# Kernel tuning notes

Measured on AMD Instinct MI355X. Metric: run time of the kernel, lower is better.

The kernel has to match this reference:

```python
import jax, jax.numpy as jnp
import numpy as np

NEG_INF = -1e30  # stand-in for -inf that is safe under fp16/bf16 softmax


def setup_inputs() -> dict:
    key = jax.random.key(0)
    k1, k2, k3, k4 = jax.random.split(key, 4)
    B, S, D_IN, D_OUT = 4, 4096, 2048, 2048
    x = jax.random.normal(k1, (B, S, D_IN), dtype=jnp.float32)
    scale = 0.02
    Wq = jax.random.normal(k2, (D_IN, D_OUT), dtype=jnp.float32) * scale
    Wk = jax.random.normal(k3, (D_IN, D_OUT), dtype=jnp.float32) * scale
    Wv = jax.random.normal(k4, (D_IN, D_OUT), dtype=jnp.float32) * scale
    return {"x": x, "Wq": Wq, "Wk": Wk, "Wv": Wv}


def reference(x, Wq, Wk, Wv):
    # x: [B, S, d_in]; Wq/Wk/Wv: [d_in, d_out] (torch Linear weight transposed)
    B, S, _ = x.shape
    q = jnp.einsum('bsd,de->bse', x, Wq)
    k = jnp.einsum('bsd,de->bse', x, Wk)
    v = jnp.einsum('bsd,de->bse', x, Wv)
    d_k = k.shape[-1]
    scale = 1.0 / jnp.sqrt(jnp.asarray(d_k, dtype=x.dtype))
    # attn_scores[b, i, j] = q_i . k_j
    scores = jnp.einsum('bqe,bke->bqk', q, k) * scale
    # causal mask: position i attends to j <= i
    i = jnp.arange(S)[:, None]
    j = jnp.arange(S)[None, :]
    scores = jnp.where(j > i, NEG_INF, scores)
    attn = jax.nn.softmax(scores, axis=-1)
    # dropout p=0.0 / eval mode -> identity
    return jnp.einsum('bqk,bke->bqe', attn, v)
```

## Files before the change

### kernel.cpp

```cpp
#include <hip/hip_runtime.h>

using u16   = unsigned short;
using s16x8 = __attribute__((ext_vector_type(8))) short;
using u16x8 = __attribute__((ext_vector_type(8))) unsigned short;
using f32x4 = __attribute__((ext_vector_type(4))) float;

__device__ __forceinline__ u16 f2bf(float f) {
    unsigned u = __float_as_uint(f);
    u += 0x7FFFu + ((u >> 16) & 1u);
    return (u16)(u >> 16);
}

__device__ __forceinline__ void gload16(const void* g, void* l) {
    __builtin_amdgcn_global_load_lds((const __attribute__((address_space(1))) void*)g,
                                     (__attribute__((address_space(3))) void*)l, 16, 0, 0);
}

#define MFMA_BF16(a, b, d) \
    d = __builtin_amdgcn_mfma_f32_16x16x32_bf16(a, b, d, 0, 0, 0)

__device__ __forceinline__ void gemm256_core(
    const u16* __restrict__ A, const u16* __restrict__ Bt,
    int lda, int ldb, int kSteps, u16* lds, f32x4 (&acc)[8][4])
{
    const int tid  = threadIdx.x;
    const int lane = tid & 63;
    const int wid  = tid >> 6;
    const int wr   = wid >> 2;
    const int wc   = wid & 3;
    const int c    = lane & 15;
    const int g    = lane >> 4;

    const int srow = tid >> 3;
    const int scol = ((tid & 7) * 8) ^ ((srow & 7) << 3);
    const u16* pA = A  + (size_t)srow * lda + scol;
    const u16* pB = Bt + (size_t)srow * ldb + scol;
    const size_t sA = (size_t)64 * lda;
    const size_t sB = (size_t)64 * ldb;
    const int ldst = tid * 8;

    const int low0 = (g * 8)      ^ ((c & 7) << 3);
    const int low1 = (32 + g * 8) ^ ((c & 7) << 3);
    const int aRow = (wr * 128 + c) * 64;
    const int bRow = (wc * 64 + c) * 64;

    {
        u16* wA = lds;
        u16* wB = lds + 16384;
        gload16(pA + 0 * sA, wA + 0 * 4096 + ldst);
        gload16(pA + 2 * sA, wA + 2 * 4096 + ldst);
        gload16(pB + 0 * sB, wB + 0 * 4096 + ldst);
        gload16(pB + 1 * sB, wB + 1 * 4096 + ldst);
        gload16(pB + 2 * sB, wB + 2 * 4096 + ldst);
        gload16(pB + 3 * sB, wB + 3 * 4096 + ldst);
        gload16(pA + 1 * sA, wA + 1 * 4096 + ldst);
        gload16(pA + 3 * sA, wA + 3 * 4096 + ldst);
    }
    if (kSteps > 1) { pA += 64; pB += 64; }

    for (int t = 0; t < kSteps; ++t) {
        const u16* rdA = lds + (t & 1) * 32768;
        const u16* rdB = rdA + 16384;
        u16* wA = lds + ((t & 1) ^ 1) * 32768;
        u16* wB = wA + 16384;
        const bool more = (t + 1 < kSteps);

        s16x8 av[4][2], bv[2][2], bw[2][2];

        asm volatile("s_waitcnt vmcnt(2)" ::: "memory");
        __builtin_amdgcn_s_barrier();
        __builtin_amdgcn_sched_barrier(0);
        if (more) {
            gload16(pA + 0 * sA, wA + 0 * 4096 + ldst);
            gload16(pA + 2 * sA, wA + 2 * 4096 + ldst);
            gload16(pB + 0 * sB, wB + 0 * 4096 + ldst);
            gload16(pB + 1 * sB, wB + 1 * 4096 + ldst);
            gload16(pB + 2 * sB, wB + 2 * 4096 + ldst);
            gload16(pB + 3 * sB, wB + 3 * 4096 + ldst);
        }
#pragma unroll
        for (int m = 0; m < 4; ++m) {
            av[m][0] = *(const s16x8*)(rdA + aRow + m * 1024 + low0);
            av[m][1] = *(const s16x8*)(rdA + aRow + m * 1024 + low1);
        }
#pragma unroll
        for (int n = 0; n < 2; ++n) {
            bv[n][0] = *(const s16x8*)(rdB + bRow + n * 1024 + low0);
            bv[n][1] = *(const s16x8*)(rdB + bRow + n * 1024 + low1);
        }
        __builtin_amdgcn_s_setprio(1);
#pragma unroll
        for (int m = 0; m < 4; ++m)
#pragma unroll
            for (int n = 0; n < 2; ++n) {
                MFMA_BF16(av[m][0], bv[n][0], acc[m][n]);
                MFMA_BF16(av[m][1], bv[n][1], acc[m][n]);
            }
        __builtin_amdgcn_s_setprio(0);
        __builtin_amdgcn_s_barrier();

#pragma unroll
        for (int n = 0; n < 2; ++n) {
            bw[n][0] = *(const s16x8*)(rdB + bRow + (n + 2) * 1024 + low0);
            bw[n][1] = *(const s16x8*)(rdB + bRow + (n + 2) * 1024 + low1);
        }
        if (more) {
            gload16(pA + 1 * sA, wA + 1 * 4096 + ldst);
            gload16(pA + 3 * sA, wA + 3 * 4096 + ldst);
        }
        __builtin_amdgcn_s_setprio(1);
#pragma unroll
        for (int m = 0; m < 4; ++m)
#pragma unroll
            for (int n = 0; n < 2; ++n) {
                MFMA_BF16(av[m][0], bw[n][0], acc[m][n + 2]);
                MFMA_BF16(av[m][1], bw[n][1], acc[m][n + 2]);
            }
        __builtin_amdgcn_s_setprio(0);

        if (more) asm volatile("s_waitcnt vmcnt(8)" ::: "memory");
        else      asm volatile("s_waitcnt vmcnt(0)" ::: "memory");
        __builtin_amdgcn_s_barrier();
        __builtin_amdgcn_sched_barrier(0);
#pragma unroll
        for (int m = 0; m < 4; ++m) {
            av[m][0] = *(const s16x8*)(rdA + aRow + (m + 4) * 1024 + low0);
            av[m][1] = *(const s16x8*)(rdA + aRow + (m + 4) * 1024 + low1);
        }
        __builtin_amdgcn_s_setprio(1);
#pragma unroll
        for (int m = 0; m < 4; ++m)
#pragma unroll
            for (int n = 0; n < 2; ++n) {
                MFMA_BF16(av[m][0], bw[n][0], acc[m + 4][n + 2]);
                MFMA_BF16(av[m][1], bw[n][1], acc[m + 4][n + 2]);
            }
        __builtin_amdgcn_s_setprio(0);
        __builtin_amdgcn_s_barrier();

        __builtin_amdgcn_s_setprio(1);
#pragma unroll
        for (int m = 0; m < 4; ++m)
#pragma unroll
            for (int n = 0; n < 2; ++n) {
                MFMA_BF16(av[m][0], bv[n][0], acc[m + 4][n]);
                MFMA_BF16(av[m][1], bv[n][1], acc[m + 4][n]);
            }
        __builtin_amdgcn_s_setprio(0);
        if (more) asm volatile("s_waitcnt vmcnt(2)" ::: "memory");
        __builtin_amdgcn_s_barrier();

        if (t + 2 < kSteps) { pA += 64; pB += 64; }
    }
    asm volatile("s_waitcnt vmcnt(0)" ::: "memory");
}

__device__ __forceinline__ int xcd_swz(int bid, int nwg) {
    return (bid & 7) * (nwg >> 3) + (bid >> 3);
}

__global__ __launch_bounds__(512, 2) void gemm256_bf16(
    const u16* __restrict__ A, const u16* __restrict__ Bt, u16* __restrict__ C,
    int N, int K, long aBatch, long bBatch, long cBatch)
{
    __shared__ u16 lds[65536];
    const int bid = xcd_swz((int)blockIdx.x, (int)gridDim.x);
    const int nT = N >> 8;
    const int m0 = (bid / nT) << 8;
    const int n0 = (bid % nT) << 8;
    const int b  = blockIdx.z;
    const u16* Ab = A  + (size_t)b * aBatch + (size_t)m0 * K;
    const u16* Bb = Bt + (size_t)b * bBatch + (size_t)n0 * K;
    f32x4 acc[8][4] = {};
    gemm256_core(Ab, Bb, K, K, K >> 6, lds, acc);

    u16* Cb = C + (size_t)b * cBatch;
    const int lane = threadIdx.x & 63;
    const int c = lane & 15, g = lane >> 4;
    const int wid = threadIdx.x >> 6;
    const int rowb = m0 + (wid >> 2) * 128 + g * 4;
    const int colb = n0 + (wid & 3) * 64 + c;
#pragma unroll
    for (int m = 0; m < 8; ++m)
#pragma unroll
        for (int n = 0; n < 4; ++n)
#pragma unroll
            for (int r = 0; r < 4; ++r)
                Cb[(size_t)(rowb + m * 16 + r) * N + colb + n * 16] = f2bf(acc[m][n][r]);
}

__global__ __launch_bounds__(512, 2) void attn_score256(
    const u16* __restrict__ Tm, const u16* __restrict__ Xb,
    u16* __restrict__ P, float* __restrict__ L, long pStride, int bBase)
{
    __shared__ u16 lds[65536];
    const int b  = bBase + blockIdx.z;
    const int wg = xcd_swz((int)blockIdx.x, (int)gridDim.x);
    int it = (int)((sqrtf(8.0f * (float)wg + 1.0f) - 1.0f) * 0.5f);
    while ((it + 1) * (it + 2) / 2 <= wg) ++it;
    while (it * (it + 1) / 2 > wg) --it;
    const int jt = wg - it * (it + 1) / 2;
    const int i0 = it << 8, j0 = jt << 8;

    const u16* Ab = Tm + ((size_t)b * 4096 + i0) * 2048;
    const u16* Bb = Xb + ((size_t)b * 4096 + j0) * 2048;
    f32x4 acc[8][4] = {};
    gemm256_core(Ab, Bb, 2048, 2048, 32, lds, acc);

    u16*   Pb = P + (size_t)blockIdx.z * pStride;
    float* Lb = L + (size_t)b * 4096;
    const int lane = threadIdx.x & 63;
    const int c = lane & 15, g = lane >> 4;
    const int wid = threadIdx.x >> 6;
    const int rowb = i0 + (wid >> 2) * 128 + g * 4;
    const int colb = j0 + (wid & 3) * 64 + c;
    const float SCALE = 0.022097086912079608f;

    float rsum[8][4];
#pragma unroll
    for (int m = 0; m < 8; ++m)
#pragma unroll
        for (int r = 0; r < 4; ++r) rsum[m][r] = 0.0f;
#pragma unroll
    for (int m = 0; m < 8; ++m) {
#pragma unroll
        for (int r = 0; r < 4; ++r) {
            const int Ig = rowb + m * 16 + r;
#pragma unroll
            for (int n = 0; n < 4; ++n) {
                const int Jg = colb + n * 16;
                float p = (Jg > Ig) ? 0.0f : __expf(acc[m][n][r] * SCALE);
                Pb[(size_t)Ig * 4096 + Jg] = f2bf(p);
                rsum[m][r] += p;
            }
        }
    }
#pragma unroll
    for (int m = 0; m < 8; ++m)
#pragma unroll
        for (int r = 0; r < 4; ++r) {
            float v = rsum[m][r];
            v += __shfl_xor(v, 1);
            v += __shfl_xor(v, 2);
            v += __shfl_xor(v, 4);
            v += __shfl_xor(v, 8);
            rsum[m][r] = v;
        }
    if (c == 0) {
#pragma unroll
        for (int m = 0; m < 8; ++m)
#pragma unroll
            for (int r = 0; r < 4; ++r)
                atomicAdd(&Lb[rowb + m * 16 + r], rsum[m][r]);
    }
}

__global__ __launch_bounds__(512, 2) void attn_pv256(
    const u16* __restrict__ P, const u16* __restrict__ Vt,
    const float* __restrict__ L, float* __restrict__ Out,
    long pStride, int bBase, int zCount)
{
    __shared__ u16 lds[65536];
    const int d = (int)blockIdx.x;
    const int x = d & 7;
    const int q = d >> 3;
    const int spr = zCount << 3;
    const int s = q % spr;
    const int r = q / spr;
    const int nt = s & 7;
    const int z  = s >> 3;
    const int it = r ? x : 15 - x;
    const int b  = bBase + z;
    const int i0 = it << 8, n0 = nt << 8;

    const u16* Ab = P  + (size_t)z * pStride + (size_t)i0 * 4096;
    const u16* Bb = Vt + (size_t)b * (2048ll * 4096) + (size_t)n0 * 4096;
    f32x4 acc[8][4] = {};
    gemm256_core(Ab, Bb, 4096, 4096, (it + 1) * 4, lds, acc);

    const float* Lb = L + (size_t)b * 4096;
    float* Ob = Out + (size_t)b * (4096ll * 2048);
    const int lane = threadIdx.x & 63;
    const int c = lane & 15, g = lane >> 4;
    const int wid = threadIdx.x >> 6;
    const int rowb = i0 + (wid >> 2) * 128 + g * 4;
    const int colb = n0 + (wid & 3) * 64 + c;
#pragma unroll
    for (int m = 0; m < 8; ++m) {
#pragma unroll
        for (int r2 = 0; r2 < 4; ++r2) {
            const int I = rowb + m * 16 + r2;
            const float inv = 1.0f / Lb[I];
#pragma unroll
            for (int n = 0; n < 4; ++n)
                Ob[(size_t)I * 2048 + colb + n * 16] = acc[m][n][r2] * inv;
        }
    }
}

__device__ __forceinline__ void gemm_core_128(
    const u16* __restrict__ A, const u16* __restrict__ Bt,
    int lda, int ldb, int kSteps,
    u16* ldsA, u16* ldsB, f32x4 (&acc)[4][4])
{
    const int tid  = threadIdx.x;
    const int lane = tid & 63;
    const int wr   = (tid >> 7) & 1;
    const int wc   = (tid >> 6) & 1;
    const int g    = lane >> 4;
    const int c    = lane & 15;

    const u16* aSrc = A  + (size_t)(tid >> 3) * lda + (tid & 7) * 8;
    const u16* bSrc = Bt + (size_t)(tid >> 3) * ldb + (tid & 7) * 8;
    u16* aDst = ldsA + tid * 8;
    u16* bDst = ldsB + tid * 8;

    for (int kt = 0; kt < kSteps; ++kt) {
#pragma unroll
        for (int it = 0; it < 4; ++it) {
            gload16(aSrc + (size_t)it * 32 * lda, aDst + it * 2048);
            gload16(bSrc + (size_t)it * 32 * ldb, bDst + it * 2048);
        }
        aSrc += 64; bSrc += 64;
        __syncthreads();
#pragma unroll
        for (int kk = 0; kk < 2; ++kk) {
            s16x8 av[4], bv[4];
#pragma unroll
            for (int m = 0; m < 4; ++m)
                av[m] = *(const s16x8*)(ldsA + (size_t)(wr*64 + m*16 + c) * 64 + kk*32 + g*8);
#pragma unroll
            for (int n = 0; n < 4; ++n)
                bv[n] = *(const s16x8*)(ldsB + (size_t)(wc*64 + n*16 + c) * 64 + kk*32 + g*8);
#pragma unroll
            for (int m = 0; m < 4; ++m)
#pragma unroll
                for (int n = 0; n < 4; ++n)
                    MFMA_BF16(av[m], bv[n], acc[m][n]);
        }
        __syncthreads();
    }
}

__global__ __launch_bounds__(256) void cvt_w2(
    const float* __restrict__ Wq, const float* __restrict__ Wk,
    u16* __restrict__ Wqb, u16* __restrict__ Wkb)
{
    int bid = (int)blockIdx.x;
    const float* src; u16* dst;
    if (bid < 2048) { src = Wq; dst = Wqb; }
    else            { src = Wk; dst = Wkb; bid -= 2048; }
    long i = (long)bid * 256 + threadIdx.x;
    const float4* p = (const float4*)(src + i * 8);
    float4 v0 = p[0], v1 = p[1];
    u16x8 o;
    o[0] = f2bf(v0.x); o[1] = f2bf(v0.y); o[2] = f2bf(v0.z); o[3] = f2bf(v0.w);
    o[4] = f2bf(v1.x); o[5] = f2bf(v1.y); o[6] = f2bf(v1.z); o[7] = f2bf(v1.w);
    *(u16x8*)(dst + i * 8) = o;
}

__global__ __launch_bounds__(256) void fused_prep(
    const float* __restrict__ x, const float* __restrict__ Wv,
    const u16* __restrict__ Wqb, const u16* __restrict__ Wkb,
    u16* __restrict__ xb, u16* __restrict__ Wvt, u16* __restrict__ Mt,
    float* __restrict__ L)
{
    __shared__ __align__(16) u16 smem[16384];
    const int bid = (int)blockIdx.x;
    const int t   = threadIdx.x;

    if (bid < 256) {
        const int m0 = (bid >> 4) << 7;
        const int n0 = (bid & 15) << 7;
        f32x4 acc[4][4] = {};
        gemm_core_128(Wkb + (size_t)m0 * 2048, Wqb + (size_t)n0 * 2048,
                      2048, 2048, 32, smem, smem + 8192, acc);
        const int lane = t & 63;
        const int wr = (t >> 7) & 1, wc = (t >> 6) & 1;
        const int rb = m0 + wr * 64 + ((lane >> 4) << 2);
        const int cb = n0 + wc * 64 + (lane & 15);
#pragma unroll
        for (int m = 0; m < 4; ++m)
#pragma unroll
            for (int n = 0; n < 4; ++n)
#pragma unroll
                for (int r = 0; r < 4; ++r)
                    Mt[(size_t)(rb + m*16 + r) * 2048 + cb + n*16] = f2bf(acc[m][n][r]);
    } else if (bid < 2304) {
        const long base = (long)(bid - 256) * 256 + t;
#pragma unroll
        for (int k = 0; k < 8; ++k) {
            const long i = base + (long)k * 524288;
            const float4* p = (const float4*)(x + i * 8);
            float4 v0 = p[0], v1 = p[1];
            u16x8 o;
            o[0] = f2bf(v0.x); o[1] = f2bf(v0.y); o[2] = f2bf(v0.z); o[3] = f2bf(v0.w);
            o[4] = f2bf(v1.x); o[5] = f2bf(v1.y); o[6] = f2bf(v1.z); o[7] = f2bf(v1.w);
            *(u16x8*)(xb + i * 8) = o;
        }
    } else if (bid < 3328) {
        float (*tile)[65] = (float (*)[65])smem;
        const int wbid = bid - 2304;
        const int br = wbid >> 5, bc = wbid & 31;
        const int lr = t >> 2;
        const int lc = (t & 3) << 4;
        const float* src = Wv + (size_t)(br * 64 + lr) * 2048 + bc * 64 + lc;
#pragma unroll
        for (int q = 0; q < 4; ++q) {
            float4 v = *(const float4*)(src + q * 4);
            tile[lr][lc + q * 4 + 0] = v.x;
            tile[lr][lc + q * 4 + 1] = v.y;
            tile[lr][lc + q * 4 + 2] = v.z;
            tile[lr][lc + q * 4 + 3] = v.w;
        }
        __syncthreads();
        u16* dst = Wvt + (size_t)(bc * 64 + lr) * 2048 + br * 64 + lc;
        u16x8 o0, o1;
#pragma unroll
        for (int q = 0; q < 8; ++q) o0[q] = f2bf(tile[lc + q][lr]);
#pragma unroll
        for (int q = 0; q < 8; ++q) o1[q] = f2bf(tile[lc + 8 + q][lr]);
        *(u16x8*)(dst)     = o0;
        *(u16x8*)(dst + 8) = o1;
    } else {
        const int i = (bid - 3328) * 256 + t;
        if (i < 16384) L[i] = 0.0f;
    }
}

extern "C" void kernel_launch(void* const* d_in, const int* in_sizes, int n_in,
                              void* d_out, int out_size, void* d_ws, size_t ws_size,
                              hipStream_t stream)
{
    const float* x  = (const float*)d_in[0];
    const float* Wq = (const float*)d_in[1];
    const float* Wk = (const float*)d_in[2];
    const float* Wv = (const float*)d_in[3];
    float* out = (float*)d_out;

    char* ws = (char*)d_ws;
    u16*   xb  = (u16*)(ws + 0ull);
    u16*   Tm  = (u16*)(ws + 67108864ull);
    u16*   Vt  = (u16*)(ws + 134217728ull);
    u16*   Wqb = (u16*)(ws + 201326592ull);
    u16*   Wkb = (u16*)(ws + 209715200ull);
    u16*   Wvt = (u16*)(ws + 218103808ull);
    u16*   Mt  = (u16*)(ws + 226492416ull);
    float* L   = (float*)(ws + 234881024ull);
    u16*   P   = (u16*)(ws + 234946560ull);
    const size_t needBase = 234946560ull;
    const size_t needFull = needBase + 134217728ull;
    const size_t needPerB = needBase + 33554432ull;
    if (ws_size < needPerB) return;

    cvt_w2<<<4096, 256, 0, stream>>>(Wq, Wk, Wqb, Wkb);
    fused_prep<<<3392, 256, 0, stream>>>(x, Wv, Wqb, Wkb, xb, Wvt, Mt, L);

    gemm256_bf16<<<dim3(512, 1, 1), 512, 0, stream>>>(xb, Mt, Tm, 2048, 2048, 0, 0, 0);
    gemm256_bf16<<<dim3(128, 1, 4), 512, 0, stream>>>(Wvt, xb, Vt, 4096, 2048,
                                                      0, 8388608, 8388608);

    if (ws_size >= needFull) {
        attn_score256<<<dim3(136, 1, 4), 512, 0, stream>>>(Tm, xb, P, L, 16777216ll, 0);
        attn_pv256   <<<dim3(512, 1, 1), 512, 0, stream>>>(P, Vt, L, out, 16777216ll, 0, 4);
    } else {
        for (int b = 0; b < 4; ++b) {
            attn_score256<<<dim3(136, 1, 1), 512, 0, stream>>>(Tm, xb, P, L, 0, b);
            attn_pv256   <<<dim3(128, 1, 1), 512, 0, stream>>>(P, Vt, L, out, 0, b, 1);
        }
    }
}
```

Measured before the change: 622.0 us.

## Use 256x128 score tiles, merge projection GEMMs, fold weight cast into prep

New measurement: 653.9 us (median of 2 runs). 5.1% more time.

```diff
diff --git a/kernel.cpp b/kernel.cpp
--- a/kernel.cpp
+++ b/kernel.cpp
@@ -18,6 +18,10 @@
 
 #define MFMA_BF16(a, b, d) \
     d = __builtin_amdgcn_mfma_f32_16x16x32_bf16(a, b, d, 0, 0, 0)
+
+__device__ __forceinline__ int xcd_swz(int bid, int nwg) {
+    return (bid & 7) * (nwg >> 3) + (bid >> 3);
+}
 
 __device__ __forceinline__ void gemm256_core(
     const u16* __restrict__ A, const u16* __restrict__ Bt,
@@ -155,26 +159,153 @@
     asm volatile("s_waitcnt vmcnt(0)" ::: "memory");
 }
 
-__device__ __forceinline__ int xcd_swz(int bid, int nwg) {
-    return (bid & 7) * (nwg >> 3) + (bid >> 3);
-}
-
-__global__ __launch_bounds__(512, 2) void gemm256_bf16(
-    const u16* __restrict__ A, const u16* __restrict__ Bt, u16* __restrict__ C,
-    int N, int K, long aBatch, long bBatch, long cBatch)
+__device__ __forceinline__ void gemm128N_core(
+    const u16* __restrict__ A, const u16* __restrict__ Bt,
+    int lda, int ldb, int kSteps, u16* lds, f32x4 (&acc)[4][4])
+{
+    const int tid  = threadIdx.x;
+    const int lane = tid & 63;
+    const int wid  = tid >> 6;
+    const int wr   = wid >> 1;
+    const int wc   = wid & 1;
+    const int c    = lane & 15;
+    const int g    = lane >> 4;
+
+    const int srow = tid >> 3;
+    const int scol = ((tid & 7) * 8) ^ ((srow & 7) << 3);
+    const u16* pA = A  + (size_t)srow * lda + scol;
+    const u16* pB = Bt + (size_t)srow * ldb + scol;
+    const size_t sA = (size_t)64 * lda;
+    const size_t sB = (size_t)64 * ldb;
+    const int ldst = tid * 8;
+
+    const int low0 = (g * 8)      ^ ((c & 7) << 3);
+    const int low1 = (32 + g * 8) ^ ((c & 7) << 3);
+    const int aRow = (wr * 64 + c) * 64;
+    const int bRow = (wc * 64 + c) * 64;
+
+    {
+        u16* wA = lds; u16* wB = lds + 16384;
+        gload16(pA + 0 * sA, wA + 0 * 4096 + ldst);
+        gload16(pA + 1 * sA, wA + 1 * 4096 + ldst);
+        gload16(pA + 2 * sA, wA + 2 * 4096 + ldst);
+        gload16(pA + 3 * sA, wA + 3 * 4096 + ldst);
+        gload16(pB + 0 * sB, wB + 0 * 4096 + ldst);
+        gload16(pB + 1 * sB, wB + 1 * 4096 + ldst);
+    }
+    if (kSteps > 1) { pA += 64; pB += 64; }
+
+    for (int t = 0; t < kSteps; ++t) {
+        const u16* rdA = lds + (t & 1) * 24576;
+        const u16* rdB = rdA + 16384;
+        u16* wA = lds + ((t & 1) ^ 1) * 24576;
+        u16* wB = wA + 16384;
+        const bool more = (t + 1 < kSteps);
+
+        s16x8 av[2][2], aw[2][2], bv[2][2], bw[2][2];
+
+        asm volatile("s_waitcnt vmcnt(0)" ::: "memory");
+        __builtin_amdgcn_s_barrier();
+        __builtin_amdgcn_sched_barrier(0);
+        if (more) {
+            gload16(pA + 0 * sA, wA + 0 * 4096 + ldst);
+            gload16(pA + 1 * sA, wA + 1 * 4096 + ldst);
+            gload16(pA + 2 * sA, wA + 2 * 4096 + ldst);
+            gload16(pA + 3 * sA, wA + 3 * 4096 + ldst);
+            gload16(pB + 0 * sB, wB + 0 * 4096 + ldst);
+            gload16(pB + 1 * sB, wB + 1 * 4096 + ldst);
+        }
+#pragma unroll
+        for (int m = 0; m < 2; ++m) {
+            av[m][0] = *(const s16x8*)(rdA + aRow + m * 1024 + low0);
+            av[m][1] = *(const s16x8*)(rdA + aRow + m * 1024 + low1);
+        }
+#pragma unroll
+        for (int n = 0; n < 2; ++n) {
+            bv[n][0] = *(const s16x8*)(rdB + bRow + n * 1024 + low0);
+            bv[n][1] = *(const s16x8*)(rdB + bRow + n * 1024 + low1);
+        }
+        __builtin_amdgcn_s_setprio(1);
+#pragma unroll
+        for (int m = 0; m < 2; ++m)
+#pragma unroll
+            for (int n = 0; n < 2; ++n) {
+                MFMA_BF16(av[m][0], bv[n][0], acc[m][n]);
+                MFMA_BF16(av[m][1], bv[n][1], acc[m][n]);
+            }
+        __builtin_amdgcn_s_setprio(0);
+        __builtin_amdgcn_s_barrier();
+
+#pragma unroll
+        for (int n = 0; n < 2; ++n) {
+            bw[n][0] = *(const s16x8*)(rdB + bRow + (n + 2) * 1024 + low0);
+            bw[n][1] = *(const s16x8*)(rdB + bRow + (n + 2) * 1024 + low1);
+        }
+        __builtin_amdgcn_s_setprio(1);
+#pragma unroll
+        for (int m = 0; m < 2; ++m)
+#pragma unroll
+            for (int n = 0; n < 2; ++n) {
+                MFMA_BF16(av[m][0], bw[n][0], acc[m][n + 2]);
+                MFMA_BF16(av[m][1], bw[n][1], acc[m][n + 2]);
+            }
+        __builtin_amdgcn_s_setprio(0);
+
+        __builtin_amdgcn_s_barrier();
+#pragma unroll
+        for (int m = 0; m < 2; ++m) {
+            aw[m][0] = *(const s16x8*)(rdA + aRow + (m + 2) * 1024 + low0);
+            aw[m][1] = *(const s16x8*)(rdA + aRow + (m + 2) * 1024 + low1);
+        }
+        __builtin_amdgcn_s_setprio(1);
+#pragma unroll
+        for (int m = 0; m < 2; ++m)
+#pragma unroll
+            for (int n = 0; n < 2; ++n) {
+                MFMA_BF16(aw[m][0], bw[n][0], acc[m + 2][n + 2]);
+                MFMA_BF16(aw[m][1], bw[n][1], acc[m + 2][n + 2]);
+            }
+        __builtin_amdgcn_s_setprio(0);
+        __builtin_amdgcn_s_barrier();
+
+        __builtin_amdgcn_s_setprio(1);
+#pragma unroll
+        for (int m = 0; m < 2; ++m)
+#pragma unroll
+            for (int n = 0; n < 2; ++n) {
+                MFMA_BF16(aw[m][0], bv[n][0], acc[m + 2][n]);
+                MFMA_BF16(aw[m][1], bv[n][1], acc[m + 2][n]);
+            }
+        __builtin_amdgcn_s_setprio(0);
+        __builtin_amdgcn_s_barrier();
+
+        if (t + 2 < kSteps) { pA += 64; pB += 64; }
+    }
+    asm volatile("s_waitcnt vmcnt(0)" ::: "memory");
+}
+
+__global__ __launch_bounds__(512, 2) void gemm256_dual(
+    const u16* __restrict__ xb, const u16* __restrict__ Mt,
+    const u16* __restrict__ Wvt, u16* __restrict__ Tm, u16* __restrict__ Vt)
 {
     __shared__ u16 lds[65536];
     const int bid = xcd_swz((int)blockIdx.x, (int)gridDim.x);
-    const int nT = N >> 8;
-    const int m0 = (bid / nT) << 8;
-    const int n0 = (bid % nT) << 8;
-    const int b  = blockIdx.z;
-    const u16* Ab = A  + (size_t)b * aBatch + (size_t)m0 * K;
-    const u16* Bb = Bt + (size_t)b * bBatch + (size_t)n0 * K;
+    const u16 *Ab, *Bb; u16* Cb; int N, m0, n0;
+    if (bid < 512) {
+        m0 = (bid >> 3) << 8; n0 = (bid & 7) << 8;
+        Ab = xb + (size_t)m0 * 2048;
+        Bb = Mt + (size_t)n0 * 2048;
+        Cb = Tm; N = 2048;
+    } else {
+        const int v = bid - 512, z = v >> 7, tile = v & 127;
+        m0 = (tile >> 4) << 8; n0 = (tile & 15) << 8;
+        Ab = Wvt + (size_t)m0 * 2048;
+        Bb = xb + (size_t)z * 8388608 + (size_t)n0 * 2048;
+        Cb = Vt + (size_t)z * 8388608; N = 4096;
+    }
     f32x4 acc[8][4] = {};
-    gemm256_core(Ab, Bb, K, K, K >> 6, lds, acc);
-
-    u16* Cb = C + (size_t)b * cBatch;
+    gemm256_core(Ab, Bb, 2048, 2048, 32, lds, acc);
+
     const int lane = threadIdx.x & 63;
     const int c = lane & 15, g = lane >> 4;
     const int wid = threadIdx.x >> 6;
@@ -189,40 +320,42 @@
                 Cb[(size_t)(rowb + m * 16 + r) * N + colb + n * 16] = f2bf(acc[m][n][r]);
 }
 
-__global__ __launch_bounds__(512, 2) void attn_score256(
+__global__ __launch_bounds__(512, 2) void attn_score128(
     const u16* __restrict__ Tm, const u16* __restrict__ Xb,
     u16* __restrict__ P, float* __restrict__ L, long pStride, int bBase)
 {
-    __shared__ u16 lds[65536];
-    const int b  = bBase + blockIdx.z;
+    __shared__ u16 lds[49152];
     const int wg = xcd_swz((int)blockIdx.x, (int)gridDim.x);
-    int it = (int)((sqrtf(8.0f * (float)wg + 1.0f) - 1.0f) * 0.5f);
-    while ((it + 1) * (it + 2) / 2 <= wg) ++it;
-    while (it * (it + 1) / 2 > wg) --it;
-    const int jt = wg - it * (it + 1) / 2;
-    const int i0 = it << 8, j0 = jt << 8;
+    const int z  = wg / 272;
+    const int j  = wg % 272;
+    const int b  = bBase + z;
+    int it = (int)((sqrtf(4.0f * (float)j + 1.0f) - 1.0f) * 0.5f);
+    while ((it + 1) * (it + 2) <= j) ++it;
+    while (it * (it + 1) > j) --it;
+    const int jt = j - it * (it + 1);
+    const int i0 = it << 8, j0 = jt << 7;
 
     const u16* Ab = Tm + ((size_t)b * 4096 + i0) * 2048;
     const u16* Bb = Xb + ((size_t)b * 4096 + j0) * 2048;
-    f32x4 acc[8][4] = {};
-    gemm256_core(Ab, Bb, 2048, 2048, 32, lds, acc);
-
-    u16*   Pb = P + (size_t)blockIdx.z * pStride;
+    f32x4 acc[4][4] = {};
+    gemm128N_core(Ab, Bb, 2048, 2048, 32, lds, acc);
+
+    u16*   Pb = P + (size_t)z * pStride;
     float* Lb = L + (size_t)b * 4096;
     const int lane = threadIdx.x & 63;
     const int c = lane & 15, g = lane >> 4;
     const int wid = threadIdx.x >> 6;
-    const int rowb = i0 + (wid >> 2) * 128 + g * 4;
-    const int colb = j0 + (wid & 3) * 64 + c;
+    const int rowb = i0 + (wid >> 1) * 64 + g * 4;
+    const int colb = j0 + (wid & 1) * 64 + c;
     const float SCALE = 0.022097086912079608f;
 
-    float rsum[8][4];
-#pragma unroll
-    for (int m = 0; m < 8; ++m)
+    float rsum[4][4];
+#pragma unroll
+    for (int m = 0; m < 4; ++m)
 #pragma unroll
         for (int r = 0; r < 4; ++r) rsum[m][r] = 0.0f;
 #pragma unroll
-    for (int m = 0; m < 8; ++m) {
+    for (int m = 0; m < 4; ++m) {
 #pragma unroll
         for (int r = 0; r < 4; ++r) {
             const int Ig = rowb + m * 16 + r;
@@ -236,7 +369,7 @@
         }
     }
 #pragma unroll
-    for (int m = 0; m < 8; ++m)
+    for (int m = 0; m < 4; ++m)
 #pragma unroll
         for (int r = 0; r < 4; ++r) {
             float v = rsum[m][r];
@@ -248,7 +381,7 @@
         }
     if (c == 0) {
 #pragma unroll
-        for (int m = 0; m < 8; ++m)
+        for (int m = 0; m < 4; ++m)
 #pragma unroll
             for (int r = 0; r < 4; ++r)
                 atomicAdd(&Lb[rowb + m * 16 + r], rsum[m][r]);
@@ -298,8 +431,8 @@
     }
 }
 
-__device__ __forceinline__ void gemm_core_128(
-    const u16* __restrict__ A, const u16* __restrict__ Bt,
+__device__ __forceinline__ void gemm_core_128_f32(
+    const float* __restrict__ A, const float* __restrict__ Bt,
     int lda, int ldb, int kSteps,
     u16* ldsA, u16* ldsB, f32x4 (&acc)[4][4])
 {
@@ -310,16 +443,24 @@
     const int g    = lane >> 4;
     const int c    = lane & 15;
 
-    const u16* aSrc = A  + (size_t)(tid >> 3) * lda + (tid & 7) * 8;
-    const u16* bSrc = Bt + (size_t)(tid >> 3) * ldb + (tid & 7) * 8;
+    const float* aSrc = A  + (size_t)(tid >> 3) * lda + (tid & 7) * 8;
+    const float* bSrc = Bt + (size_t)(tid >> 3) * ldb + (tid & 7) * 8;
     u16* aDst = ldsA + tid * 8;
     u16* bDst = ldsB + tid * 8;
 
     for (int kt = 0; kt < kSteps; ++kt) {
 #pragma unroll
         for (int it = 0; it < 4; ++it) {
-            gload16(aSrc + (size_t)it * 32 * lda, aDst + it * 2048);
-            gload16(bSrc + (size_t)it * 32 * ldb, bDst + it * 2048);
+            const float4* pa = (const float4*)(aSrc + (size_t)it * 32 * lda);
+            const float4* pb = (const float4*)(bSrc + (size_t)it * 32 * ldb);
+            float4 a0 = pa[0], a1 = pa[1], b0 = pb[0], b1 = pb[1];
+            u16x8 oa, ob;
+            oa[0]=f2bf(a0.x); oa[1]=f2bf(a0.y); oa[2]=f2bf(a0.z); oa[3]=f2bf(a0.w);
+            oa[4]=f2bf(a1.x); oa[5]=f2bf(a1.y); oa[6]=f2bf(a1.z); oa[7]=f2bf(a1.w);
+            ob[0]=f2bf(b0.x); ob[1]=f2bf(b0.y); ob[2]=f2bf(b0.z); ob[3]=f2bf(b0.w);
+            ob[4]=f2bf(b1.x); ob[5]=f2bf(b1.y); ob[6]=f2bf(b1.z); ob[7]=f2bf(b1.w);
+            *(u16x8*)(aDst + it * 2048) = oa;
+            *(u16x8*)(bDst + it * 2048) = ob;
         }
         aSrc += 64; bSrc += 64;
         __syncthreads();
@@ -342,26 +483,9 @@
     }
 }
 
-__global__ __launch_bounds__(256) void cvt_w2(
-    const float* __restrict__ Wq, const float* __restrict__ Wk,
-    u16* __restrict__ Wqb, u16* __restrict__ Wkb)
-{
-    int bid = (int)blockIdx.x;
-    const float* src; u16* dst;
-    if (bid < 2048) { src = Wq; dst = Wqb; }
-    else            { src = Wk; dst = Wkb; bid -= 2048; }
-    long i = (long)bid * 256 + threadIdx.x;
-    const float4* p = (const float4*)(src + i * 8);
-    float4 v0 = p[0], v1 = p[1];
-    u16x8 o;
-    o[0] = f2bf(v0.x); o[1] = f2bf(v0.y); o[2] = f2bf(v0.z); o[3] = f2bf(v0.w);
-    o[4] = f2bf(v1.x); o[5] = f2bf(v1.y); o[6] = f2bf(v1.z); o[7] = f2bf(v1.w);
-    *(u16x8*)(dst + i * 8) = o;
-}
-
 __global__ __launch_bounds__(256) void fused_prep(
     const float* __restrict__ x, const float* __restrict__ Wv,
-    const u16* __restrict__ Wqb, const u16* __restrict__ Wkb,
+    const float* __restrict__ Wq, const float* __restrict__ Wk,
     u16* __restrict__ xb, u16* __restrict__ Wvt, u16* __restrict__ Mt,
     float* __restrict__ L)
 {
@@ -373,8 +497,8 @@
         const int m0 = (bid >> 4) << 7;
         const int n0 = (bid & 15) << 7;
         f32x4 acc[4][4] = {};
-        gemm_core_128(Wkb + (size_t)m0 * 2048, Wqb + (size_t)n0 * 2048,
-                      2048, 2048, 32, smem, smem + 8192, acc);
+        gemm_core_128_f32(Wk + (size_t)m0 * 2048, Wq + (size_t)n0 * 2048,
+                          2048, 2048, 32, smem, smem + 8192, acc);
         const int lane = t & 63;
         const int wr = (t >> 7) & 1, wc = (t >> 6) & 1;
         const int rb = m0 + wr * 64 + ((lane >> 4) << 2);
@@ -442,8 +566,6 @@
     u16*   xb  = (u16*)(ws + 0ull);
     u16*   Tm  = (u16*)(ws + 67108864ull);
     u16*   Vt  = (u16*)(ws + 134217728ull);
-    u16*   Wqb = (u16*)(ws + 201326592ull);
-    u16*   Wkb = (u16*)(ws + 209715200ull);
     u16*   Wvt = (u16*)(ws + 218103808ull);
     u16*   Mt  = (u16*)(ws + 226492416ull);
     float* L   = (float*)(ws + 234881024ull);
@@ -453,20 +575,17 @@
     const size_t needPerB = needBase + 33554432ull;
     if (ws_size < needPerB) return;
 
-    cvt_w2<<<4096, 256, 0, stream>>>(Wq, Wk, Wqb, Wkb);
-    fused_prep<<<3392, 256, 0, stream>>>(x, Wv, Wqb, Wkb, xb, Wvt, Mt, L);
-
-    gemm256_bf16<<<dim3(512, 1, 1), 512, 0, stream>>>(xb, Mt, Tm, 2048, 2048, 0, 0, 0);
-    gemm256_bf16<<<dim3(128, 1, 4), 512, 0, stream>>>(Wvt, xb, Vt, 4096, 2048,
-                                                      0, 8388608, 8388608);
+    fused_prep<<<3392, 256, 0, stream>>>(x, Wv, Wq, Wk, xb, Wvt, Mt, L);
+
+    gemm256_dual<<<1024, 512, 0, stream>>>(xb, Mt, Wvt, Tm, Vt);
 
     if (ws_size >= needFull) {
-        attn_score256<<<dim3(136, 1, 4), 512, 0, stream>>>(Tm, xb, P, L, 16777216ll, 0);
-        attn_pv256   <<<dim3(512, 1, 1), 512, 0, stream>>>(P, Vt, L, out, 16777216ll, 0, 4);
+        attn_score128<<<1088, 512, 0, stream>>>(Tm, xb, P, L, 16777216ll, 0);
+        attn_pv256   <<<512,  512, 0, stream>>>(P, Vt, L, out, 16777216ll, 0, 4);
     } else {
         for (int b = 0; b < 4; ++b) {
-            attn_score256<<<dim3(136, 1, 1), 512, 0, stream>>>(Tm, xb, P, L, 0, b);
-            attn_pv256   <<<dim3(128, 1, 1), 512, 0, stream>>>(P, Vt, L, out, 0, b, 1);
-        }
-    }
-}
+            attn_score128<<<272, 512, 0, stream>>>(Tm, xb, P, L, 0, b);
+            attn_pv256   <<<128, 512, 0, stream>>>(P, Vt, L, out, 0, b, 1);
+        }
+    }
+}
```

## Flatten score grid, group causal tiles into 4x4 blocks, use exp2

Applied to the files above, without the earlier changes.

After: 631.1 us. No clear change (+1.5%).

```diff
diff --git a/kernel.cpp b/kernel.cpp
--- a/kernel.cpp
+++ b/kernel.cpp
@@ -191,15 +191,30 @@
 
 __global__ __launch_bounds__(512, 2) void attn_score256(
     const u16* __restrict__ Tm, const u16* __restrict__ Xb,
-    u16* __restrict__ P, float* __restrict__ L, long pStride, int bBase)
+    u16* __restrict__ P, float* __restrict__ L, long pStride, int bBase,
+    int perBatch)
 {
     __shared__ u16 lds[65536];
-    const int b  = bBase + blockIdx.z;
     const int wg = xcd_swz((int)blockIdx.x, (int)gridDim.x);
-    int it = (int)((sqrtf(8.0f * (float)wg + 1.0f) - 1.0f) * 0.5f);
-    while ((it + 1) * (it + 2) / 2 <= wg) ++it;
-    while (it * (it + 1) / 2 > wg) --it;
-    const int jt = wg - it * (it + 1) / 2;
+    const int z  = perBatch ? 0 : (wg / 136);
+    const int j  = perBatch ? wg : (wg % 136);
+    const int b  = bBase + z;
+
+    int it, jt;
+    if (j < 40) {
+        const int p = j / 10, cc = j % 10;
+        const int di = (cc >= 6) ? 3 : (cc >= 3) ? 2 : (cc >= 1) ? 1 : 0;
+        const int dj = cc - ((di * (di + 1)) >> 1);
+        it = 4 * p + di;
+        jt = 4 * p + dj;
+    } else {
+        const int jj = j - 40;
+        const int p  = jj >> 4, cc = jj & 15;
+        const int ip = (p >= 3) ? 3 : (p >= 1) ? 2 : 1;
+        const int jp = p - ((ip * (ip - 1)) >> 1);
+        it = 4 * ip + (cc >> 2);
+        jt = 4 * jp + (cc & 3);
+    }
     const int i0 = it << 8, j0 = jt << 8;
 
     const u16* Ab = Tm + ((size_t)b * 4096 + i0) * 2048;
@@ -207,14 +222,14 @@
     f32x4 acc[8][4] = {};
     gemm256_core(Ab, Bb, 2048, 2048, 32, lds, acc);
 
-    u16*   Pb = P + (size_t)blockIdx.z * pStride;
+    u16*   Pb = P + (size_t)z * pStride;
     float* Lb = L + (size_t)b * 4096;
     const int lane = threadIdx.x & 63;
     const int c = lane & 15, g = lane >> 4;
     const int wid = threadIdx.x >> 6;
     const int rowb = i0 + (wid >> 2) * 128 + g * 4;
     const int colb = j0 + (wid & 3) * 64 + c;
-    const float SCALE = 0.022097086912079608f;
+    const float SC2 = 0.022097086912079608f * 1.4426950408889634f;
 
     float rsum[8][4];
 #pragma unroll
@@ -229,7 +244,7 @@
 #pragma unroll
             for (int n = 0; n < 4; ++n) {
                 const int Jg = colb + n * 16;
-                float p = (Jg > Ig) ? 0.0f : __expf(acc[m][n][r] * SCALE);
+                float p = (Jg > Ig) ? 0.0f : exp2f(acc[m][n][r] * SC2);
                 Pb[(size_t)Ig * 4096 + Jg] = f2bf(p);
                 rsum[m][r] += p;
             }
@@ -346,17 +361,20 @@
     const float* __restrict__ Wq, const float* __restrict__ Wk,
     u16* __restrict__ Wqb, u16* __restrict__ Wkb)
 {
-    int bid = (int)blockIdx.x;
-    const float* src; u16* dst;
-    if (bid < 2048) { src = Wq; dst = Wqb; }
-    else            { src = Wk; dst = Wkb; bid -= 2048; }
-    long i = (long)bid * 256 + threadIdx.x;
-    const float4* p = (const float4*)(src + i * 8);
-    float4 v0 = p[0], v1 = p[1];
-    u16x8 o;
-    o[0] = f2bf(v0.x); o[1] = f2bf(v0.y); o[2] = f2bf(v0.z); o[3] = f2bf(v0.w);
-    o[4] = f2bf(v1.x); o[5] = f2bf(v1.y); o[6] = f2bf(v1.z); o[7] = f2bf(v1.w);
-    *(u16x8*)(dst + i * 8) = o;
+    const long base = (long)blockIdx.x * 256 + threadIdx.x;
+#pragma unroll
+    for (int k = 0; k < 4; ++k) {
+        const long i = base + (long)k * 262144;
+        const float* src = (k < 2) ? Wq : Wk;
+        u16*         dst = (k < 2) ? Wqb : Wkb;
+        const long off = (k < 2) ? i : (i - 524288);
+        const float4* p = (const float4*)(src + off * 8);
+        float4 v0 = p[0], v1 = p[1];
+        u16x8 o;
+        o[0] = f2bf(v0.x); o[1] = f2bf(v0.y); o[2] = f2bf(v0.z); o[3] = f2bf(v0.w);
+        o[4] = f2bf(v1.x); o[5] = f2bf(v1.y); o[6] = f2bf(v1.z); o[7] = f2bf(v1.w);
+        *(u16x8*)(dst + off * 8) = o;
+    }
 }
 
 __global__ __launch_bounds__(256) void fused_prep(
@@ -453,7 +471,7 @@
     const size_t needPerB = needBase + 33554432ull;
     if (ws_size < needPerB) return;
 
-    cvt_w2<<<4096, 256, 0, stream>>>(Wq, Wk, Wqb, Wkb);
+    cvt_w2<<<1024, 256, 0, stream>>>(Wq, Wk, Wqb, Wkb);
     fused_prep<<<3392, 256, 0, stream>>>(x, Wv, Wqb, Wkb, xb, Wvt, Mt, L);
 
     gemm256_bf16<<<dim3(512, 1, 1), 512, 0, stream>>>(xb, Mt, Tm, 2048, 2048, 0, 0, 0);
@@ -461,11 +479,11 @@
                                                       0, 8388608, 8388608);
 
     if (ws_size >= needFull) {
-        attn_score256<<<dim3(136, 1, 4), 512, 0, stream>>>(Tm, xb, P, L, 16777216ll, 0);
+        attn_score256<<<dim3(544, 1, 1), 512, 0, stream>>>(Tm, xb, P, L, 16777216ll, 0, 0);
         attn_pv256   <<<dim3(512, 1, 1), 512, 0, stream>>>(P, Vt, L, out, 16777216ll, 0, 4);
     } else {
         for (int b = 0; b < 4; ++b) {
-            attn_score256<<<dim3(136, 1, 1), 512, 0, stream>>>(Tm, xb, P, L, 0, b);
+            attn_score256<<<dim3(136, 1, 1), 512, 0, stream>>>(Tm, xb, P, L, 0, b, 1);
             attn_pv256   <<<dim3(128, 1, 1), 512, 0, stream>>>(P, Vt, L, out, 0, b, 1);
         }
     }
```
